# Optimization experiments

Hardware: AMD Instinct MI355X
Metric: run time of the kernel (lower is better)

The kernel has to match this reference:

```python
import jax, jax.numpy as jnp
import numpy as np

K = 3
NUM_STEP_COMBO = 5
BN_EPS = 1e-5


def setup_inputs() -> dict:
    key = jax.random.key(0)
    ks = jax.random.split(key, 10)
    N, E, D, H, O, G = 100000, 1600000, 48, 128, 12, 64
    x = jax.random.normal(ks[0], (N, D), dtype=jnp.float32)
    edge_index = jax.random.randint(ks[1], (2, E), 0, N, dtype=jnp.int64)
    batch = jnp.sort(jax.random.randint(ks[2], (N,), 0, G, dtype=jnp.int64))
    # ChebConv params: one [D, D] weight per Chebyshev order, shared bias
    W = jax.random.normal(ks[3], (K, D, D), dtype=jnp.float32) * 0.1
    b = jnp.zeros((D,), dtype=jnp.float32)
    gamma = jnp.ones((D,), dtype=jnp.float32)
    beta = jnp.zeros((D,), dtype=jnp.float32)
    W1 = jax.random.normal(ks[4], (D, H), dtype=jnp.float32) * 0.1
    b1 = jnp.zeros((H,), dtype=jnp.float32)
    W2 = jax.random.normal(ks[5], (H, O), dtype=jnp.float32) * 0.1
    b2 = jnp.zeros((O,), dtype=jnp.float32)
    return {"x": x, "edge_index": edge_index, "batch": batch, "num_graphs": 64,
            "W": W, "b": b, "gamma": gamma, "beta": beta,
            "W1": W1, "b1": b1, "W2": W2, "b2": b2}


def cheb_conv(x, row, col, W, b):
    # PyG ChebConv, sym norm, lambda_max=2 => L_hat = -D^{-1/2} A D^{-1/2}
    N = x.shape[0]
    deg = jax.ops.segment_sum(jnp.ones_like(row, dtype=x.dtype), row, num_segments=N)
    dinv = jnp.where(deg > 0, jax.lax.rsqrt(jnp.maximum(deg, 1.0)), 0.0)
    norm = (-dinv[row] * dinv[col])[:, None]  # [E,1] edge weights of L_hat

    def lhat(v):  # sparse matvec: gather neighbors, scale, scatter-add
        return jax.ops.segment_sum(norm * v[col], row, num_segments=N)

    Tx0 = x
    Tx1 = lhat(x)
    out = Tx0 @ W[0] + Tx1 @ W[1]
    Txkm2, Txkm1 = Tx0, Tx1
    for k in range(2, W.shape[0]):
        Txk = 2.0 * lhat(Txkm1) - Txkm2
        out = out + Txk @ W[k]
        Txkm2, Txkm1 = Txkm1, Txk
    return out + b


def reference(x, edge_index, batch, num_graphs, W, b, gamma, beta, W1, b1, W2, b2):
    row, col = edge_index[0], edge_index[1]
    N = x.shape[0]
    out = x
    for _ in range(NUM_STEP_COMBO):
        t = jax.nn.relu(cheb_conv(out, row, col, W, b))
        # BatchNorm1d (training-mode stats over all nodes, biased var)
        mean = jnp.mean(t, axis=0)
        var = jnp.mean((t - mean) ** 2, axis=0)
        t = gamma * (t - mean) * jax.lax.rsqrt(var + BN_EPS) + beta
        # graph_max_pool: per-node max over incoming neighbor features
        m = jax.ops.segment_max(t[col], row, num_segments=N)
        out = jnp.where(jnp.isneginf(m), 0.0, m)  # empty segments -> 0
    g = jax.ops.segment_sum(out, batch, num_segments=num_graphs)  # global_add_pool
    h = jax.nn.relu(g @ W1 + b1)
    return h @ W2 + b2
```

## Files before the change

### kernel.cpp

```cpp
#include <hip/hip_runtime.h>
#include <hip/hip_bf16.h>

#define D 48
#define GNUM 64
#define HDIM 128
#define ODIM 12
#define BN_EPS 1e-5f

typedef _Float16 half4v __attribute__((ext_vector_type(4)));
typedef float f32x4 __attribute__((ext_vector_type(4)));

#define MFMA16(a, b, c) __builtin_amdgcn_mfma_f32_16x16x16f16((a), (b), (c), 0, 0, 0)


__global__ __launch_bounds__(256) void k_deg(const int* __restrict__ row, int* __restrict__ deg, int E) {
    int e = blockIdx.x * 256 + threadIdx.x;
    if (e < E) atomicAdd(&deg[row[e]], 1);
}

__global__ __launch_bounds__(256) void k_scan1(const int* __restrict__ deg, int* __restrict__ incl,
                                               int* __restrict__ bsum, float* __restrict__ dinv, int N) {
    __shared__ int s[256];
    int i = blockIdx.x * 256 + threadIdx.x;
    int d = (i < N) ? deg[i] : 0;
    if (i < N) dinv[i] = d > 0 ? rsqrtf((float)d) : 0.f;
    s[threadIdx.x] = d;
    __syncthreads();
    for (int off = 1; off < 256; off <<= 1) {
        int t = (threadIdx.x >= off) ? s[threadIdx.x - off] : 0;
        __syncthreads();
        s[threadIdx.x] += t;
        __syncthreads();
    }
    if (i < N) incl[i] = s[threadIdx.x];
    if (threadIdx.x == 255) bsum[blockIdx.x] = s[255];
}

__global__ __launch_bounds__(512) void k_scan2(int* __restrict__ bsum, int nb) {
    __shared__ int s[512];
    int t = threadIdx.x;
    s[t] = (t < nb) ? bsum[t] : 0;
    __syncthreads();
    for (int off = 1; off < 512; off <<= 1) {
        int v = (t >= off) ? s[t - off] : 0;
        __syncthreads();
        s[t] += v;
        __syncthreads();
    }
    if (t < nb) bsum[t] = s[t];
}

__global__ __launch_bounds__(256) void k_scan3(const int* __restrict__ incl, const int* __restrict__ bsum,
                                               int* __restrict__ rowptr, int N) {
    int i = blockIdx.x * 256 + threadIdx.x;
    if (i < N) {
        int add = (blockIdx.x > 0) ? bsum[blockIdx.x - 1] : 0;
        rowptr[i + 1] = incl[i] + add;
    }
    if (i == 0) rowptr[0] = 0;
}

__global__ __launch_bounds__(256) void k_fill(const int* __restrict__ row, const int* __restrict__ col,
                                              const int* __restrict__ rowptr, int* __restrict__ fillc,
                                              const float* __restrict__ dinv, int2* __restrict__ epair,
                                              int E, int N) {
    int part = blockIdx.x & 7;
    int sub = blockIdx.x >> 3;
    int nsub = (int)(gridDim.x >> 3);
    int lo = (int)(((long long)N * part) >> 3);
    int hi = (int)(((long long)N * (part + 1)) >> 3);
    for (int e = sub * 256 + threadIdx.x; e < E; e += nsub * 256) {
        int r = __builtin_nontemporal_load(&row[e]);
        if (r >= lo && r < hi) {
            int c = __builtin_nontemporal_load(&col[e]);
            int p = rowptr[r] + atomicAdd(&fillc[r], 1);
            epair[p] = make_int2(c, __float_as_int(dinv[c]));
        }
    }
}

__global__ __launch_bounds__(256) void k_cvt(const float* __restrict__ x, _Float16* __restrict__ xh, int n4) {
    int i = blockIdx.x * 256 + threadIdx.x;
    if (i < n4) {
        float4 v = ((const float4*)x)[i];
        half4v h;
        h.x = (_Float16)v.x; h.y = (_Float16)v.y; h.z = (_Float16)v.z; h.w = (_Float16)v.w;
        ((half4v*)xh)[i] = h;
    }
}

__global__ __launch_bounds__(256) void k_wb(const float* __restrict__ W, _Float16* __restrict__ WB) {
    int idx = blockIdx.x * 256 + threadIdx.x;
    if (idx < 27 * 64) {
        int lane = idx & 63, ct = idx >> 6;
        int c = ct / 3, tl = ct % 3;
        int col = lane & 15, kg = lane >> 4;
        half4v h;
#pragma unroll
        for (int j = 0; j < 4; ++j) h[j] = (_Float16)W[(c * 16 + kg * 4 + j) * 48 + tl * 16 + col];
        *(half4v*)(WB + (size_t)idx * 4) = h;
    }
}


__global__ __launch_bounds__(256) void k_lhat(const _Float16* __restrict__ cur, const int* __restrict__ rowptr,
                                              const int2* __restrict__ epair, const float* __restrict__ dinv,
                                              _Float16* __restrict__ tx1, int N) {
    int lane = threadIdx.x & 63;
    int i = (blockIdx.x * 256 + threadIdx.x) >> 6;
    if (i >= N) return;
    int q = lane & 15, slot = lane >> 4;
    int qc = q < 12 ? q : 11;
    int s = rowptr[i], e = rowptr[i + 1];
    float a0 = 0.f, a1 = 0.f, a2 = 0.f, a3 = 0.f;
    int p = s + slot;
    for (; p + 12 < e; p += 16) {
        int2 e0 = epair[p], e1 = epair[p + 4], e2 = epair[p + 8], e3 = epair[p + 12];
        half4v h0 = *(const half4v*)(cur + (size_t)e0.x * D + qc * 4);
        half4v h1 = *(const half4v*)(cur + (size_t)e1.x * D + qc * 4);
        half4v h2 = *(const half4v*)(cur + (size_t)e2.x * D + qc * 4);
        half4v h3 = *(const half4v*)(cur + (size_t)e3.x * D + qc * 4);
        float w0 = __int_as_float(e0.y), w1 = __int_as_float(e1.y);
        float w2 = __int_as_float(e2.y), w3 = __int_as_float(e3.y);
        a0 += w0 * (float)h0.x + w1 * (float)h1.x + w2 * (float)h2.x + w3 * (float)h3.x;
        a1 += w0 * (float)h0.y + w1 * (float)h1.y + w2 * (float)h2.y + w3 * (float)h3.y;
        a2 += w0 * (float)h0.z + w1 * (float)h1.z + w2 * (float)h2.z + w3 * (float)h3.z;
        a3 += w0 * (float)h0.w + w1 * (float)h1.w + w2 * (float)h2.w + w3 * (float)h3.w;
    }
    for (; p < e; p += 4) {
        int2 ea = epair[p];
        float wa = __int_as_float(ea.y);
        half4v ha = *(const half4v*)(cur + (size_t)ea.x * D + qc * 4);
        a0 += wa * (float)ha.x; a1 += wa * (float)ha.y; a2 += wa * (float)ha.z; a3 += wa * (float)ha.w;
    }
    a0 += __shfl_xor(a0, 16); a1 += __shfl_xor(a1, 16); a2 += __shfl_xor(a2, 16); a3 += __shfl_xor(a3, 16);
    a0 += __shfl_xor(a0, 32); a1 += __shfl_xor(a1, 32); a2 += __shfl_xor(a2, 32); a3 += __shfl_xor(a3, 32);
    if (lane < 12) {
        float sc = -dinv[i];
        half4v o;
        o.x = (_Float16)(sc * a0); o.y = (_Float16)(sc * a1);
        o.z = (_Float16)(sc * a2); o.w = (_Float16)(sc * a3);
        *(half4v*)(tx1 + (size_t)i * D + lane * 4) = o;
    }
}

__global__ __launch_bounds__(256) void k_gather2(const _Float16* __restrict__ tx0, const _Float16* __restrict__ tx1,
                                                 const int* __restrict__ rowptr, const int2* __restrict__ epair,
                                                 const float* __restrict__ dinv, _Float16* __restrict__ tx2, int N) {
    int lane = threadIdx.x & 63;
    int i = (blockIdx.x * 256 + threadIdx.x) >> 6;
    if (i >= N) return;
    int q = lane & 15, slot = lane >> 4;
    int qc = q < 12 ? q : 11;
    int s = rowptr[i], e = rowptr[i + 1];
    float a0 = 0.f, a1 = 0.f, a2 = 0.f, a3 = 0.f;
    int p = s + slot;
    for (; p + 12 < e; p += 16) {
        int2 e0 = epair[p], e1 = epair[p + 4], e2 = epair[p + 8], e3 = epair[p + 12];
        half4v h0 = *(const half4v*)(tx1 + (size_t)e0.x * D + qc * 4);
        half4v h1 = *(const half4v*)(tx1 + (size_t)e1.x * D + qc * 4);
        half4v h2 = *(const half4v*)(tx1 + (size_t)e2.x * D + qc * 4);
        half4v h3 = *(const half4v*)(tx1 + (size_t)e3.x * D + qc * 4);
        float w0 = __int_as_float(e0.y), w1 = __int_as_float(e1.y);
        float w2 = __int_as_float(e2.y), w3 = __int_as_float(e3.y);
        a0 += w0 * (float)h0.x + w1 * (float)h1.x + w2 * (float)h2.x + w3 * (float)h3.x;
        a1 += w0 * (float)h0.y + w1 * (float)h1.y + w2 * (float)h2.y + w3 * (float)h3.y;
        a2 += w0 * (float)h0.z + w1 * (float)h1.z + w2 * (float)h2.z + w3 * (float)h3.z;
        a3 += w0 * (float)h0.w + w1 * (float)h1.w + w2 * (float)h2.w + w3 * (float)h3.w;
    }
    for (; p < e; p += 4) {
        int2 ea = epair[p];
        float wa = __int_as_float(ea.y);
        half4v ha = *(const half4v*)(tx1 + (size_t)ea.x * D + qc * 4);
        a0 += wa * (float)ha.x; a1 += wa * (float)ha.y; a2 += wa * (float)ha.z; a3 += wa * (float)ha.w;
    }
    a0 += __shfl_xor(a0, 16); a1 += __shfl_xor(a1, 16); a2 += __shfl_xor(a2, 16); a3 += __shfl_xor(a3, 16);
    a0 += __shfl_xor(a0, 32); a1 += __shfl_xor(a1, 32); a2 += __shfl_xor(a2, 32); a3 += __shfl_xor(a3, 32);
    if (lane < 12) {
        float sc = -2.f * dinv[i];
        half4v h0 = *(const half4v*)(tx0 + (size_t)i * D + lane * 4);
        half4v o;
        o.x = (_Float16)(sc * a0 - (float)h0.x); o.y = (_Float16)(sc * a1 - (float)h0.y);
        o.z = (_Float16)(sc * a2 - (float)h0.z); o.w = (_Float16)(sc * a3 - (float)h0.w);
        *(half4v*)(tx2 + (size_t)i * D + lane * 4) = o;
    }
}


__global__ __launch_bounds__(256) void k_dense(const _Float16* __restrict__ tx0, const _Float16* __restrict__ tx1,
                                               const _Float16* __restrict__ tx2, const _Float16* __restrict__ WB,
                                               const float* __restrict__ b, _Float16* __restrict__ tbuf,
                                               float* __restrict__ bnst, int N) {
    __shared__ float bns[2 * D];
    int t = threadIdx.x;
    if (t < 2 * D) bns[t] = 0.f;
    __syncthreads();

    int lane = t & 63, wave = t >> 6;
    int node0 = (blockIdx.x * 4 + wave) * 16;
    if (node0 < N) {
        int col = lane & 15, kg = lane >> 4;
        int nodeA = node0 + col;
        bool inA = nodeA < N;
        const _Float16* __restrict__ Xs[3] = {tx0 + (size_t)nodeA * D, tx1 + (size_t)nodeA * D,
                                              tx2 + (size_t)nodeA * D};
        f32x4 acc0 = {}, acc1 = {}, acc2 = {};
#pragma unroll
        for (int c = 0; c < 9; ++c) {
            half4v a = {};
            if (inA) a = *(const half4v*)(Xs[c / 3] + (c % 3) * 16 + kg * 4);
            half4v b0 = *(const half4v*)(WB + ((size_t)(c * 3 + 0) * 64 + lane) * 4);
            half4v b1 = *(const half4v*)(WB + ((size_t)(c * 3 + 1) * 64 + lane) * 4);
            half4v b2 = *(const half4v*)(WB + ((size_t)(c * 3 + 2) * 64 + lane) * 4);
            acc0 = MFMA16(a, b0, acc0);
            acc1 = MFMA16(a, b1, acc1);
            acc2 = MFMA16(a, b2, acc2);
        }
        float bc0 = b[col], bc1 = b[16 + col], bc2 = b[32 + col];
        float s0 = 0.f, q0 = 0.f, s1 = 0.f, q1 = 0.f, s2 = 0.f, q2 = 0.f;
#pragma unroll
        for (int i = 0; i < 4; ++i) {
            int nd = node0 + kg * 4 + i;
            float v0 = fmaxf(acc0[i] + bc0, 0.f);
            float v1 = fmaxf(acc1[i] + bc1, 0.f);
            float v2 = fmaxf(acc2[i] + bc2, 0.f);
            if (nd < N) {
                _Float16* o = tbuf + (size_t)nd * D;
                o[col] = (_Float16)v0;
                o[16 + col] = (_Float16)v1;
                o[32 + col] = (_Float16)v2;
                s0 += v0; q0 += v0 * v0;
                s1 += v1; q1 += v1 * v1;
                s2 += v2; q2 += v2 * v2;
            }
        }
        s0 += __shfl_xor(s0, 16); s0 += __shfl_xor(s0, 32);
        q0 += __shfl_xor(q0, 16); q0 += __shfl_xor(q0, 32);
        s1 += __shfl_xor(s1, 16); s1 += __shfl_xor(s1, 32);
        q1 += __shfl_xor(q1, 16); q1 += __shfl_xor(q1, 32);
        s2 += __shfl_xor(s2, 16); s2 += __shfl_xor(s2, 32);
        q2 += __shfl_xor(q2, 16); q2 += __shfl_xor(q2, 32);
        if (lane < 16) {
            atomicAdd(&bns[col], s0);      atomicAdd(&bns[D + col], q0);
            atomicAdd(&bns[16 + col], s1); atomicAdd(&bns[D + 16 + col], q1);
            atomicAdd(&bns[32 + col], s2); atomicAdd(&bns[D + 32 + col], q2);
        }
    }
    __syncthreads();
    if (t < 2 * D) atomicAdd(&bnst[t], bns[t]);
}


__global__ __launch_bounds__(256) void k_pool(const _Float16* __restrict__ tbuf, const int* __restrict__ rowptr,
                                              const int2* __restrict__ epair, const float* __restrict__ bnst,
                                              const float* __restrict__ gamma, const float* __restrict__ beta,
                                              float Ninv, _Float16* __restrict__ outh, int N) {
    __shared__ float ssL[2 * D];
    int t = threadIdx.x;
    if (t < D) {
        float mean = bnst[t] * Ninv;
        float var = fmaxf(bnst[D + t] * Ninv - mean * mean, 0.f);
        float sc = gamma[t] * rsqrtf(var + BN_EPS);
        ssL[t] = sc;
        ssL[D + t] = beta[t] - mean * sc;
    }
    __syncthreads();
    int lane = t & 63;
    int i = (blockIdx.x * 256 + t) >> 6;
    if (i >= N) return;
    int q = lane & 15, slot = lane >> 4;
    int qc = q < 12 ? q : 11;
    int s = rowptr[i], e = rowptr[i + 1];
    float m0 = -3.4e38f, m1 = -3.4e38f, m2 = -3.4e38f, m3 = -3.4e38f;
    float n0 = 3.4e38f, n1 = 3.4e38f, n2 = 3.4e38f, n3 = 3.4e38f;
    int p = s + slot;
    for (; p + 12 < e; p += 16) {
        int c0 = epair[p].x, c1 = epair[p + 4].x, c2 = epair[p + 8].x, c3 = epair[p + 12].x;
        half4v h0 = *(const half4v*)(tbuf + (size_t)c0 * D + qc * 4);
        half4v h1 = *(const half4v*)(tbuf + (size_t)c1 * D + qc * 4);
        half4v h2 = *(const half4v*)(tbuf + (size_t)c2 * D + qc * 4);
        half4v h3 = *(const half4v*)(tbuf + (size_t)c3 * D + qc * 4);
        float x00 = (float)h0.x, x01 = (float)h0.y, x02 = (float)h0.z, x03 = (float)h0.w;
        float x10 = (float)h1.x, x11 = (float)h1.y, x12 = (float)h1.z, x13 = (float)h1.w;
        float x20 = (float)h2.x, x21 = (float)h2.y, x22 = (float)h2.z, x23 = (float)h2.w;
        float x30 = (float)h3.x, x31 = (float)h3.y, x32 = (float)h3.z, x33 = (float)h3.w;
        m0 = fmaxf(m0, fmaxf(fmaxf(x00, x10), fmaxf(x20, x30)));
        m1 = fmaxf(m1, fmaxf(fmaxf(x01, x11), fmaxf(x21, x31)));
        m2 = fmaxf(m2, fmaxf(fmaxf(x02, x12), fmaxf(x22, x32)));
        m3 = fmaxf(m3, fmaxf(fmaxf(x03, x13), fmaxf(x23, x33)));
        n0 = fminf(n0, fminf(fminf(x00, x10), fminf(x20, x30)));
        n1 = fminf(n1, fminf(fminf(x01, x11), fminf(x21, x31)));
        n2 = fminf(n2, fminf(fminf(x02, x12), fminf(x22, x32)));
        n3 = fminf(n3, fminf(fminf(x03, x13), fminf(x23, x33)));
    }
    for (; p < e; p += 4) {
        int ca = epair[p].x;
        half4v ha = *(const half4v*)(tbuf + (size_t)ca * D + qc * 4);
        float a0 = (float)ha.x, a1 = (float)ha.y, a2 = (float)ha.z, a3 = (float)ha.w;
        m0 = fmaxf(m0, a0); m1 = fmaxf(m1, a1); m2 = fmaxf(m2, a2); m3 = fmaxf(m3, a3);
        n0 = fminf(n0, a0); n1 = fminf(n1, a1); n2 = fminf(n2, a2); n3 = fminf(n3, a3);
    }
    m0 = fmaxf(m0, __shfl_xor(m0, 16)); m1 = fmaxf(m1, __shfl_xor(m1, 16));
    m2 = fmaxf(m2, __shfl_xor(m2, 16)); m3 = fmaxf(m3, __shfl_xor(m3, 16));
    m0 = fmaxf(m0, __shfl_xor(m0, 32)); m1 = fmaxf(m1, __shfl_xor(m1, 32));
    m2 = fmaxf(m2, __shfl_xor(m2, 32)); m3 = fmaxf(m3, __shfl_xor(m3, 32));
    n0 = fminf(n0, __shfl_xor(n0, 16)); n1 = fminf(n1, __shfl_xor(n1, 16));
    n2 = fminf(n2, __shfl_xor(n2, 16)); n3 = fminf(n3, __shfl_xor(n3, 16));
    n0 = fminf(n0, __shfl_xor(n0, 32)); n1 = fminf(n1, __shfl_xor(n1, 32));
    n2 = fminf(n2, __shfl_xor(n2, 32)); n3 = fminf(n3, __shfl_xor(n3, 32));
    if (lane < 12) {
        float4 sc = *(const float4*)(ssL + lane * 4);
        float4 sh = *(const float4*)(ssL + D + lane * 4);
        half4v o;
        if (s == e) {
            o.x = (_Float16)0.f; o.y = (_Float16)0.f; o.z = (_Float16)0.f; o.w = (_Float16)0.f;
        } else {
            float v0 = (sc.x >= 0.f) ? sc.x * m0 + sh.x : sc.x * n0 + sh.x;
            float v1 = (sc.y >= 0.f) ? sc.y * m1 + sh.y : sc.y * n1 + sh.y;
            float v2 = (sc.z >= 0.f) ? sc.z * m2 + sh.z : sc.z * n2 + sh.z;
            float v3 = (sc.w >= 0.f) ? sc.w * m3 + sh.w : sc.w * n3 + sh.w;
            o.x = (_Float16)v0; o.y = (_Float16)v1; o.z = (_Float16)v2; o.w = (_Float16)v3;
        }
        *(half4v*)(outh + (size_t)i * D + lane * 4) = o;
    }
}


__global__ __launch_bounds__(256) void k_gpool(const _Float16* __restrict__ outh, const int* __restrict__ batch,
                                               float* __restrict__ g, int N, int chunk) {
    int lane = threadIdx.x & 63;
    int wid = (blockIdx.x * 256 + threadIdx.x) >> 6;
    int start = wid * chunk;
    if (start >= N || lane >= 12) return;
    int end = start + chunk;
    if (end > N) end = N;
    int curb = batch[start];
    float a0 = 0.f, a1 = 0.f, a2 = 0.f, a3 = 0.f;
    for (int i = start; i < end; ++i) {
        int bi = batch[i];
        if (bi != curb) {
            atomicAdd(&g[curb * D + lane * 4 + 0], a0); atomicAdd(&g[curb * D + lane * 4 + 1], a1);
            atomicAdd(&g[curb * D + lane * 4 + 2], a2); atomicAdd(&g[curb * D + lane * 4 + 3], a3);
            curb = bi; a0 = a1 = a2 = a3 = 0.f;
        }
        half4v h = *(const half4v*)(outh + (size_t)i * D + lane * 4);
        a0 += (float)h.x; a1 += (float)h.y; a2 += (float)h.z; a3 += (float)h.w;
    }
    atomicAdd(&g[curb * D + lane * 4 + 0], a0); atomicAdd(&g[curb * D + lane * 4 + 1], a1);
    atomicAdd(&g[curb * D + lane * 4 + 2], a2); atomicAdd(&g[curb * D + lane * 4 + 3], a3);
}

__global__ __launch_bounds__(256) void k_mlp(const float* __restrict__ g, const float* __restrict__ W1,
                                             const float* __restrict__ b1, const float* __restrict__ W2,
                                             const float* __restrict__ b2, float* __restrict__ out) {
    __shared__ float gL[GNUM * D];
    __shared__ float hL[GNUM * HDIM];
    __shared__ float W1L[D * HDIM];
    int t = threadIdx.x;
    for (int i = t; i < GNUM * D; i += 256) gL[i] = g[i];
    for (int i = t; i < D * HDIM; i += 256) W1L[i] = W1[i];
    __syncthreads();
    for (int i = t; i < GNUM * HDIM; i += 256) {
        int gi = i >> 7, hj = i & 127;
        float a = b1[hj];
        for (int k = 0; k < D; ++k) a += gL[gi * D + k] * W1L[k * HDIM + hj];
        hL[i] = fmaxf(a, 0.f);
    }
    __syncthreads();
    for (int i = t; i < GNUM * ODIM; i += 256) {
        int gi = i / ODIM, oj = i % ODIM;
        float a = b2[oj];
        for (int k = 0; k < HDIM; ++k) a += hL[gi * HDIM + k] * W2[k * ODIM + oj];
        out[i] = a;
    }
}


extern "C" void kernel_launch(void* const* d_in, const int* in_sizes, int n_in,
                              void* d_out, int out_size, void* d_ws, size_t ws_size,
                              hipStream_t stream) {
    const float* x     = (const float*)d_in[0];
    const int*   ei    = (const int*)d_in[1];
    const int*   batch = (const int*)d_in[2];
    const float* W     = (const float*)d_in[4];
    const float* b     = (const float*)d_in[5];
    const float* gamma = (const float*)d_in[6];
    const float* beta  = (const float*)d_in[7];
    const float* W1    = (const float*)d_in[8];
    const float* b1    = (const float*)d_in[9];
    const float* W2    = (const float*)d_in[10];
    const float* b2    = (const float*)d_in[11];

    int N = in_sizes[0] / D;
    int E = in_sizes[1] / 2;
    const int* row = ei;
    const int* col = ei + E;

    char* w = (char*)d_ws;
    auto alloc = [&](size_t bytes) { char* p = w; w += (bytes + 255) & ~(size_t)255; return p; };
    int*       deg     = (int*)alloc((size_t)N * 4);
    float*     dinv    = (float*)alloc((size_t)N * 4);
    int*       fillc   = (int*)alloc((size_t)N * 4);
    int*       incl    = (int*)alloc((size_t)N * 4);
    int*       bsum    = (int*)alloc(4096);
    int*       rowptr  = (int*)alloc((size_t)(N + 1) * 4);
    int2*      epair   = (int2*)alloc((size_t)E * 8);
    _Float16*  xh      = (_Float16*)alloc((size_t)N * D * 2 + 64);
    _Float16*  tx1h    = (_Float16*)alloc((size_t)N * D * 2 + 64);
    _Float16*  tx2h    = (_Float16*)alloc((size_t)N * D * 2 + 64);
    _Float16*  tbufh   = (_Float16*)alloc((size_t)N * D * 2 + 64);
    _Float16*  outh    = (_Float16*)alloc((size_t)N * D * 2 + 64);
    _Float16*  WB      = (_Float16*)alloc(27 * 64 * 4 * 2);
    float*     bnstats = (float*)alloc(5 * 2 * D * 4);
    float*     g       = (float*)alloc((size_t)GNUM * D * 4);

    (void)hipMemsetAsync(deg, 0, (size_t)N * 4, stream);
    (void)hipMemsetAsync(fillc, 0, (size_t)N * 4, stream);
    (void)hipMemsetAsync(bnstats, 0, 5 * 2 * D * 4, stream);
    (void)hipMemsetAsync(g, 0, (size_t)GNUM * D * 4, stream);

    int nbE = (E + 255) / 256;
    int nbN = (N + 255) / 256;

    k_deg<<<nbE, 256, 0, stream>>>(row, deg, E);
    k_scan1<<<nbN, 256, 0, stream>>>(deg, incl, bsum, dinv, N);
    k_scan2<<<1, 512, 0, stream>>>(bsum, nbN);
    k_scan3<<<nbN, 256, 0, stream>>>(incl, bsum, rowptr, N);
    k_fill<<<2048, 256, 0, stream>>>(row, col, rowptr, fillc, dinv, epair, E, N);
    int n4 = N * D / 4;
    k_cvt<<<(n4 + 255) / 256, 256, 0, stream>>>(x, xh, n4);
    k_wb<<<7, 256, 0, stream>>>(W, WB);

    int nbWave = (N * 64 + 255) / 256;
    int nbDense = (((N + 15) / 16) + 3) / 4;
    float Ninv = 1.f / (float)N;
    const _Float16* cur = xh;
    for (int step = 0; step < 5; ++step) {
        float* bnst = bnstats + step * 2 * D;
        k_lhat<<<nbWave, 256, 0, stream>>>(cur, rowptr, epair, dinv, tx1h, N);
        k_gather2<<<nbWave, 256, 0, stream>>>(cur, tx1h, rowptr, epair, dinv, tx2h, N);
        k_dense<<<nbDense, 256, 0, stream>>>(cur, tx1h, tx2h, WB, b, tbufh, bnst, N);
        k_pool<<<nbWave, 256, 0, stream>>>(tbufh, rowptr, epair, bnst, gamma, beta, Ninv, outh, N);
        cur = outh;
    }

    int chunk = 32;
    int nwaves = (N + chunk - 1) / chunk;
    int nbG = (nwaves * 64 + 255) / 256;
    k_gpool<<<nbG, 256, 0, stream>>>(outh, batch, g, N, chunk);
    k_mlp<<<1, 256, 0, stream>>>(g, W1, b1, W2, b2, (float*)d_out);
}
```

Measured before the change: 1.342 ms.

## Build CSR via bucketed two-pass scatter instead of 8-way partitioned fill

```diff
diff --git a/kernel.cpp b/kernel.cpp
--- a/kernel.cpp
+++ b/kernel.cpp
@@ -60,22 +60,69 @@
     if (i == 0) rowptr[0] = 0;
 }
 
-__global__ __launch_bounds__(256) void k_fill(const int* __restrict__ row, const int* __restrict__ col,
-                                              const int* __restrict__ rowptr, int* __restrict__ fillc,
-                                              const float* __restrict__ dinv, int2* __restrict__ epair,
-                                              int E, int N) {
+
+__global__ __launch_bounds__(256) void k_bcnt(const int* __restrict__ row, int* __restrict__ bcnt, int E) {
+    __shared__ int h[256];
+    h[threadIdx.x] = 0;
+    __syncthreads();
     int part = blockIdx.x & 7;
-    int sub = blockIdx.x >> 3;
-    int nsub = (int)(gridDim.x >> 3);
-    int lo = (int)(((long long)N * part) >> 3);
-    int hi = (int)(((long long)N * (part + 1)) >> 3);
-    for (int e = sub * 256 + threadIdx.x; e < E; e += nsub * 256) {
-        int r = __builtin_nontemporal_load(&row[e]);
-        if (r >= lo && r < hi) {
-            int c = __builtin_nontemporal_load(&col[e]);
-            int p = rowptr[r] + atomicAdd(&fillc[r], 1);
-            epair[p] = make_int2(c, __float_as_int(dinv[c]));
-        }
+    for (int e = blockIdx.x * 256 + threadIdx.x; e < E; e += gridDim.x * 256)
+        atomicAdd(&h[row[e] >> 9], 1);
+    __syncthreads();
+    int c = h[threadIdx.x];
+    if (c) atomicAdd(&bcnt[(threadIdx.x << 3) | part], c);
+}
+
+__global__ __launch_bounds__(512) void k_bscan(const int* __restrict__ bcnt, int* __restrict__ bstart,
+                                               int* __restrict__ bfill, int M) {
+    __shared__ int s[512];
+    int t = threadIdx.x;
+    int vals[4];
+    int acc = 0;
+#pragma unroll
+    for (int k = 0; k < 4; ++k) {
+        int i = t * 4 + k;
+        vals[k] = (i < M) ? bcnt[i] : 0;
+        acc += vals[k];
+    }
+    s[t] = acc;
+    __syncthreads();
+    for (int off = 1; off < 512; off <<= 1) {
+        int v = (t >= off) ? s[t - off] : 0;
+        __syncthreads();
+        s[t] += v;
+        __syncthreads();
+    }
+    int ex = s[t] - acc;
+#pragma unroll
+    for (int k = 0; k < 4; ++k) {
+        int i = t * 4 + k;
+        if (i < M) { bstart[i] = ex; bfill[i] = ex; }
+        ex += vals[k];
+    }
+}
+
+__global__ __launch_bounds__(256) void k_bscat(const int* __restrict__ row, const int* __restrict__ col,
+                                               int* __restrict__ bfill, int2* __restrict__ ebuf, int E) {
+    int part = blockIdx.x & 7;
+    for (int e = blockIdx.x * 256 + threadIdx.x; e < E; e += gridDim.x * 256) {
+        int r = row[e], c = col[e];
+        int pos = atomicAdd(&bfill[((r >> 9) << 3) | part], 1);
+        ebuf[pos] = make_int2(r, c);
+    }
+}
+
+__global__ __launch_bounds__(256) void k_cfill(const int2* __restrict__ ebuf, const int* __restrict__ rowptr,
+                                               int* __restrict__ fillc, const float* __restrict__ dinv,
+                                               int2* __restrict__ epair, int E) {
+    int part = blockIdx.x >> 8;
+    int sub = blockIdx.x & 255;
+    int lo = (int)((long long)E * part / 8);
+    int hi = (int)((long long)E * (part + 1) / 8);
+    for (int e = lo + sub * 256 + threadIdx.x; e < hi; e += 256 * 256) {
+        int2 rc = ebuf[e];
+        int pos = rowptr[rc.x] + atomicAdd(&fillc[rc.x], 1);
+        epair[pos] = make_int2(rc.y, __float_as_int(dinv[rc.y]));
     }
 }
 
@@ -404,6 +451,9 @@
     int*       incl    = (int*)alloc((size_t)N * 4);
     int*       bsum    = (int*)alloc(4096);
     int*       rowptr  = (int*)alloc((size_t)(N + 1) * 4);
+    int*       bcnt    = (int*)alloc(2048 * 4);
+    int*       bstart  = (int*)alloc(2048 * 4);
+    int*       bfill   = (int*)alloc(2048 * 4);
     int2*      epair   = (int2*)alloc((size_t)E * 8);
     _Float16*  xh      = (_Float16*)alloc((size_t)N * D * 2 + 64);
     _Float16*  tx1h    = (_Float16*)alloc((size_t)N * D * 2 + 64);
@@ -413,20 +463,27 @@
     _Float16*  WB      = (_Float16*)alloc(27 * 64 * 4 * 2);
     float*     bnstats = (float*)alloc(5 * 2 * D * 4);
     float*     g       = (float*)alloc((size_t)GNUM * D * 4);
+    int2*      ebuf    = (int2*)tbufh;
 
     (void)hipMemsetAsync(deg, 0, (size_t)N * 4, stream);
     (void)hipMemsetAsync(fillc, 0, (size_t)N * 4, stream);
+    (void)hipMemsetAsync(bcnt, 0, 2048 * 4, stream);
     (void)hipMemsetAsync(bnstats, 0, 5 * 2 * D * 4, stream);
     (void)hipMemsetAsync(g, 0, (size_t)GNUM * D * 4, stream);
 
     int nbE = (E + 255) / 256;
     int nbN = (N + 255) / 256;
+    int NB = (N + 511) >> 9;
+    int M = NB * 8;
 
     k_deg<<<nbE, 256, 0, stream>>>(row, deg, E);
     k_scan1<<<nbN, 256, 0, stream>>>(deg, incl, bsum, dinv, N);
     k_scan2<<<1, 512, 0, stream>>>(bsum, nbN);
     k_scan3<<<nbN, 256, 0, stream>>>(incl, bsum, rowptr, N);
-    k_fill<<<2048, 256, 0, stream>>>(row, col, rowptr, fillc, dinv, epair, E, N);
+    k_bcnt<<<2048, 256, 0, stream>>>(row, bcnt, E);
+    k_bscan<<<1, 512, 0, stream>>>(bcnt, bstart, bfill, M);
+    k_bscat<<<2048, 256, 0, stream>>>(row, col, bfill, ebuf, E);
+    k_cfill<<<2048, 256, 0, stream>>>(ebuf, rowptr, fillc, dinv, epair, E);
     int n4 = N * D / 4;
     k_cvt<<<(n4 + 255) / 256, 256, 0, stream>>>(x, xh, n4);
     k_wb<<<7, 256, 0, stream>>>(W, WB);
```

Measured after the change: 1.619 ms. 20.6% more time.

## Widen gather loads to 16-byte half8 with 8 edge slots per wave

Applied to the files above, without the earlier changes.

```diff
diff --git a/kernel.cpp b/kernel.cpp
--- a/kernel.cpp
+++ b/kernel.cpp
@@ -8,6 +8,7 @@
 #define BN_EPS 1e-5f
 
 typedef _Float16 half4v __attribute__((ext_vector_type(4)));
+typedef _Float16 half8v __attribute__((ext_vector_type(8)));
 typedef float f32x4 __attribute__((ext_vector_type(4)));
 
 #define MFMA16(a, b, c) __builtin_amdgcn_mfma_f32_16x16x16f16((a), (b), (c), 0, 0, 0)
@@ -63,16 +64,16 @@
 __global__ __launch_bounds__(256) void k_fill(const int* __restrict__ row, const int* __restrict__ col,
                                               const int* __restrict__ rowptr, int* __restrict__ fillc,
                                               const float* __restrict__ dinv, int2* __restrict__ epair,
-                                              int E, int N) {
+                                              int e0, int e1, int N) {
     int part = blockIdx.x & 7;
     int sub = blockIdx.x >> 3;
     int nsub = (int)(gridDim.x >> 3);
     int lo = (int)(((long long)N * part) >> 3);
     int hi = (int)(((long long)N * (part + 1)) >> 3);
-    for (int e = sub * 256 + threadIdx.x; e < E; e += nsub * 256) {
-        int r = __builtin_nontemporal_load(&row[e]);
+    for (int e = e0 + sub * 256 + threadIdx.x; e < e1; e += nsub * 256) {
+        int r = row[e];
         if (r >= lo && r < hi) {
-            int c = __builtin_nontemporal_load(&col[e]);
+            int c = col[e];
             int p = rowptr[r] + atomicAdd(&fillc[r], 1);
             epair[p] = make_int2(c, __float_as_int(dinv[c]));
         }
@@ -103,44 +104,61 @@
 }
 
 
+#define GATHER_REDUCE8(A)                                             \
+    A##0 += __shfl_xor(A##0, 8);  A##1 += __shfl_xor(A##1, 8);        \
+    A##2 += __shfl_xor(A##2, 8);  A##3 += __shfl_xor(A##3, 8);        \
+    A##4 += __shfl_xor(A##4, 8);  A##5 += __shfl_xor(A##5, 8);        \
+    A##6 += __shfl_xor(A##6, 8);  A##7 += __shfl_xor(A##7, 8);        \
+    A##0 += __shfl_xor(A##0, 16); A##1 += __shfl_xor(A##1, 16);       \
+    A##2 += __shfl_xor(A##2, 16); A##3 += __shfl_xor(A##3, 16);       \
+    A##4 += __shfl_xor(A##4, 16); A##5 += __shfl_xor(A##5, 16);       \
+    A##6 += __shfl_xor(A##6, 16); A##7 += __shfl_xor(A##7, 16);       \
+    A##0 += __shfl_xor(A##0, 32); A##1 += __shfl_xor(A##1, 32);       \
+    A##2 += __shfl_xor(A##2, 32); A##3 += __shfl_xor(A##3, 32);       \
+    A##4 += __shfl_xor(A##4, 32); A##5 += __shfl_xor(A##5, 32);       \
+    A##6 += __shfl_xor(A##6, 32); A##7 += __shfl_xor(A##7, 32);
+
 __global__ __launch_bounds__(256) void k_lhat(const _Float16* __restrict__ cur, const int* __restrict__ rowptr,
                                               const int2* __restrict__ epair, const float* __restrict__ dinv,
                                               _Float16* __restrict__ tx1, int N) {
     int lane = threadIdx.x & 63;
     int i = (blockIdx.x * 256 + threadIdx.x) >> 6;
     if (i >= N) return;
-    int q = lane & 15, slot = lane >> 4;
-    int qc = q < 12 ? q : 11;
+    int slot = lane >> 3, j = lane & 7;
+    int jb = (j < 6 ? j : 5) * 8;
     int s = rowptr[i], e = rowptr[i + 1];
-    float a0 = 0.f, a1 = 0.f, a2 = 0.f, a3 = 0.f;
+    float a0 = 0.f, a1 = 0.f, a2 = 0.f, a3 = 0.f, a4 = 0.f, a5 = 0.f, a6 = 0.f, a7 = 0.f;
     int p = s + slot;
-    for (; p + 12 < e; p += 16) {
-        int2 e0 = epair[p], e1 = epair[p + 4], e2 = epair[p + 8], e3 = epair[p + 12];
-        half4v h0 = *(const half4v*)(cur + (size_t)e0.x * D + qc * 4);
-        half4v h1 = *(const half4v*)(cur + (size_t)e1.x * D + qc * 4);
-        half4v h2 = *(const half4v*)(cur + (size_t)e2.x * D + qc * 4);
-        half4v h3 = *(const half4v*)(cur + (size_t)e3.x * D + qc * 4);
-        float w0 = __int_as_float(e0.y), w1 = __int_as_float(e1.y);
-        float w2 = __int_as_float(e2.y), w3 = __int_as_float(e3.y);
-        a0 += w0 * (float)h0.x + w1 * (float)h1.x + w2 * (float)h2.x + w3 * (float)h3.x;
-        a1 += w0 * (float)h0.y + w1 * (float)h1.y + w2 * (float)h2.y + w3 * (float)h3.y;
-        a2 += w0 * (float)h0.z + w1 * (float)h1.z + w2 * (float)h2.z + w3 * (float)h3.z;
-        a3 += w0 * (float)h0.w + w1 * (float)h1.w + w2 * (float)h2.w + w3 * (float)h3.w;
-    }
-    for (; p < e; p += 4) {
+    for (; p + 8 < e; p += 16) {
+        int2 ea = epair[p], eb = epair[p + 8];
+        half8v ha = *(const half8v*)(cur + (size_t)ea.x * D + jb);
+        half8v hb = *(const half8v*)(cur + (size_t)eb.x * D + jb);
+        float wa = __int_as_float(ea.y), wb = __int_as_float(eb.y);
+        a0 += wa * (float)ha[0] + wb * (float)hb[0];
+        a1 += wa * (float)ha[1] + wb * (float)hb[1];
+        a2 += wa * (float)ha[2] + wb * (float)hb[2];
+        a3 += wa * (float)ha[3] + wb * (float)hb[3];
+        a4 += wa * (float)ha[4] + wb * (float)hb[4];
+        a5 += wa * (float)ha[5] + wb * (float)hb[5];
+        a6 += wa * (float)ha[6] + wb * (float)hb[6];
+        a7 += wa * (float)ha[7] + wb * (float)hb[7];
+    }
+    if (p < e) {
         int2 ea = epair[p];
+        half8v ha = *(const half8v*)(cur + (size_t)ea.x * D + jb);
         float wa = __int_as_float(ea.y);
-        half4v ha = *(const half4v*)(cur + (size_t)ea.x * D + qc * 4);
-        a0 += wa * (float)ha.x; a1 += wa * (float)ha.y; a2 += wa * (float)ha.z; a3 += wa * (float)ha.w;
-    }
-    a0 += __shfl_xor(a0, 16); a1 += __shfl_xor(a1, 16); a2 += __shfl_xor(a2, 16); a3 += __shfl_xor(a3, 16);
-    a0 += __shfl_xor(a0, 32); a1 += __shfl_xor(a1, 32); a2 += __shfl_xor(a2, 32); a3 += __shfl_xor(a3, 32);
-    if (lane < 12) {
+        a0 += wa * (float)ha[0]; a1 += wa * (float)ha[1]; a2 += wa * (float)ha[2]; a3 += wa * (float)ha[3];
+        a4 += wa * (float)ha[4]; a5 += wa * (float)ha[5]; a6 += wa * (float)ha[6]; a7 += wa * (float)ha[7];
+    }
+    GATHER_REDUCE8(a)
+    if (slot == 0 && j < 6) {
         float sc = -dinv[i];
-        half4v o;
-        o.x = (_Float16)(sc * a0); o.y = (_Float16)(sc * a1);
-        o.z = (_Float16)(sc * a2); o.w = (_Float16)(sc * a3);
-        *(half4v*)(tx1 + (size_t)i * D + lane * 4) = o;
+        half8v o;
+        o[0] = (_Float16)(sc * a0); o[1] = (_Float16)(sc * a1);
+        o[2] = (_Float16)(sc * a2); o[3] = (_Float16)(sc * a3);
+        o[4] = (_Float16)(sc * a4); o[5] = (_Float16)(sc * a5);
+        o[6] = (_Float16)(sc * a6); o[7] = (_Float16)(sc * a7);
+        *(half8v*)(tx1 + (size_t)i * D + jb) = o;
     }
 }
 
@@ -150,39 +168,42 @@
     int lane = threadIdx.x & 63;
     int i = (blockIdx.x * 256 + threadIdx.x) >> 6;
     if (i >= N) return;
-    int q = lane & 15, slot = lane >> 4;
-    int qc = q < 12 ? q : 11;
+    int slot = lane >> 3, j = lane & 7;
+    int jb = (j < 6 ? j : 5) * 8;
     int s = rowptr[i], e = rowptr[i + 1];
-    float a0 = 0.f, a1 = 0.f, a2 = 0.f, a3 = 0.f;
+    float a0 = 0.f, a1 = 0.f, a2 = 0.f, a3 = 0.f, a4 = 0.f, a5 = 0.f, a6 = 0.f, a7 = 0.f;
     int p = s + slot;
-    for (; p + 12 < e; p += 16) {
-        int2 e0 = epair[p], e1 = epair[p + 4], e2 = epair[p + 8], e3 = epair[p + 12];
-        half4v h0 = *(const half4v*)(tx1 + (size_t)e0.x * D + qc * 4);
-        half4v h1 = *(const half4v*)(tx1 + (size_t)e1.x * D + qc * 4);
-        half4v h2 = *(const half4v*)(tx1 + (size_t)e2.x * D + qc * 4);
-        half4v h3 = *(const half4v*)(tx1 + (size_t)e3.x * D + qc * 4);
-        float w0 = __int_as_float(e0.y), w1 = __int_as_float(e1.y);
-        float w2 = __int_as_float(e2.y), w3 = __int_as_float(e3.y);
-        a0 += w0 * (float)h0.x + w1 * (float)h1.x + w2 * (float)h2.x + w3 * (float)h3.x;
-        a1 += w0 * (float)h0.y + w1 * (float)h1.y + w2 * (float)h2.y + w3 * (float)h3.y;
-        a2 += w0 * (float)h0.z + w1 * (float)h1.z + w2 * (float)h2.z + w3 * (float)h3.z;
-        a3 += w0 * (float)h0.w + w1 * (float)h1.w + w2 * (float)h2.w + w3 * (float)h3.w;
-    }
-    for (; p < e; p += 4) {
+    for (; p + 8 < e; p += 16) {
+        int2 ea = epair[p], eb = epair[p + 8];
+        half8v ha = *(const half8v*)(tx1 + (size_t)ea.x * D + jb);
+        half8v hb = *(const half8v*)(tx1 + (size_t)eb.x * D + jb);
+        float wa = __int_as_float(ea.y), wb = __int_as_float(eb.y);
+        a0 += wa * (float)ha[0] + wb * (float)hb[0];
+        a1 += wa * (float)ha[1] + wb * (float)hb[1];
+        a2 += wa * (float)ha[2] + wb * (float)hb[2];
+        a3 += wa * (float)ha[3] + wb * (float)hb[3];
+        a4 += wa * (float)ha[4] + wb * (float)hb[4];
+        a5 += wa * (float)ha[5] + wb * (float)hb[5];
+        a6 += wa * (float)ha[6] + wb * (float)hb[6];
+        a7 += wa * (float)ha[7] + wb * (float)hb[7];
+    }
+    if (p < e) {
         int2 ea = epair[p];
+        half8v ha = *(const half8v*)(tx1 + (size_t)ea.x * D + jb);
         float wa = __int_as_float(ea.y);
-        half4v ha = *(const half4v*)(tx1 + (size_t)ea.x * D + qc * 4);
-        a0 += wa * (float)ha.x; a1 += wa * (float)ha.y; a2 += wa * (float)ha.z; a3 += wa * (float)ha.w;
-    }
-    a0 += __shfl_xor(a0, 16); a1 += __shfl_xor(a1, 16); a2 += __shfl_xor(a2, 16); a3 += __shfl_xor(a3, 16);
-    a0 += __shfl_xor(a0, 32); a1 += __shfl_xor(a1, 32); a2 += __shfl_xor(a2, 32); a3 += __shfl_xor(a3, 32);
-    if (lane < 12) {
+        a0 += wa * (float)ha[0]; a1 += wa * (float)ha[1]; a2 += wa * (float)ha[2]; a3 += wa * (float)ha[3];
+        a4 += wa * (float)ha[4]; a5 += wa * (float)ha[5]; a6 += wa * (float)ha[6]; a7 += wa * (float)ha[7];
+    }
+    GATHER_REDUCE8(a)
+    if (slot == 0 && j < 6) {
         float sc = -2.f * dinv[i];
-        half4v h0 = *(const half4v*)(tx0 + (size_t)i * D + lane * 4);
-        half4v o;
-        o.x = (_Float16)(sc * a0 - (float)h0.x); o.y = (_Float16)(sc * a1 - (float)h0.y);
-        o.z = (_Float16)(sc * a2 - (float)h0.z); o.w = (_Float16)(sc * a3 - (float)h0.w);
-        *(half4v*)(tx2 + (size_t)i * D + lane * 4) = o;
+        half8v h0 = *(const half8v*)(tx0 + (size_t)i * D + jb);
+        half8v o;
+        o[0] = (_Float16)(sc * a0 - (float)h0[0]); o[1] = (_Float16)(sc * a1 - (float)h0[1]);
+        o[2] = (_Float16)(sc * a2 - (float)h0[2]); o[3] = (_Float16)(sc * a3 - (float)h0[3]);
+        o[4] = (_Float16)(sc * a4 - (float)h0[4]); o[5] = (_Float16)(sc * a5 - (float)h0[5]);
+        o[6] = (_Float16)(sc * a6 - (float)h0[6]); o[7] = (_Float16)(sc * a7 - (float)h0[7]);
+        *(half8v*)(tx2 + (size_t)i * D + jb) = o;
     }
 }
 
@@ -268,60 +289,73 @@
     int lane = t & 63;
     int i = (blockIdx.x * 256 + t) >> 6;
     if (i >= N) return;
-    int q = lane & 15, slot = lane >> 4;
-    int qc = q < 12 ? q : 11;
+    int slot = lane >> 3, j = lane & 7;
+    int jb = (j < 6 ? j : 5) * 8;
     int s = rowptr[i], e = rowptr[i + 1];
     float m0 = -3.4e38f, m1 = -3.4e38f, m2 = -3.4e38f, m3 = -3.4e38f;
+    float m4 = -3.4e38f, m5 = -3.4e38f, m6 = -3.4e38f, m7 = -3.4e38f;
     float n0 = 3.4e38f, n1 = 3.4e38f, n2 = 3.4e38f, n3 = 3.4e38f;
+    float n4 = 3.4e38f, n5 = 3.4e38f, n6 = 3.4e38f, n7 = 3.4e38f;
     int p = s + slot;
-    for (; p + 12 < e; p += 16) {
-        int c0 = epair[p].x, c1 = epair[p + 4].x, c2 = epair[p + 8].x, c3 = epair[p + 12].x;
-        half4v h0 = *(const half4v*)(tbuf + (size_t)c0 * D + qc * 4);
-        half4v h1 = *(const half4v*)(tbuf + (size_t)c1 * D + qc * 4);
-        half4v h2 = *(const half4v*)(tbuf + (size_t)c2 * D + qc * 4);
-        half4v h3 = *(const half4v*)(tbuf + (size_t)c3 * D + qc * 4);
-        float x00 = (float)h0.x, x01 = (float)h0.y, x02 = (float)h0.z, x03 = (float)h0.w;
-        float x10 = (float)h1.x, x11 = (float)h1.y, x12 = (float)h1.z, x13 = (float)h1.w;
-        float x20 = (float)h2.x, x21 = (float)h2.y, x22 = (float)h2.z, x23 = (float)h2.w;
-        float x30 = (float)h3.x, x31 = (float)h3.y, x32 = (float)h3.z, x33 = (float)h3.w;
-        m0 = fmaxf(m0, fmaxf(fmaxf(x00, x10), fmaxf(x20, x30)));
-        m1 = fmaxf(m1, fmaxf(fmaxf(x01, x11), fmaxf(x21, x31)));
-        m2 = fmaxf(m2, fmaxf(fmaxf(x02, x12), fmaxf(x22, x32)));
-        m3 = fmaxf(m3, fmaxf(fmaxf(x03, x13), fmaxf(x23, x33)));
-        n0 = fminf(n0, fminf(fminf(x00, x10), fminf(x20, x30)));
-        n1 = fminf(n1, fminf(fminf(x01, x11), fminf(x21, x31)));
-        n2 = fminf(n2, fminf(fminf(x02, x12), fminf(x22, x32)));
-        n3 = fminf(n3, fminf(fminf(x03, x13), fminf(x23, x33)));
-    }
-    for (; p < e; p += 4) {
+    for (; p + 8 < e; p += 16) {
+        int ca = epair[p].x, cb = epair[p + 8].x;
+        half8v ha = *(const half8v*)(tbuf + (size_t)ca * D + jb);
+        half8v hb = *(const half8v*)(tbuf + (size_t)cb * D + jb);
+        float x0 = (float)ha[0], y0 = (float)hb[0], x1 = (float)ha[1], y1 = (float)hb[1];
+        float x2 = (float)ha[2], y2 = (float)hb[2], x3 = (float)ha[3], y3 = (float)hb[3];
+        float x4 = (float)ha[4], y4 = (float)hb[4], x5 = (float)ha[5], y5 = (float)hb[5];
+        float x6 = (float)ha[6], y6 = (float)hb[6], x7 = (float)ha[7], y7 = (float)hb[7];
+        m0 = fmaxf(m0, fmaxf(x0, y0)); m1 = fmaxf(m1, fmaxf(x1, y1));
+        m2 = fmaxf(m2, fmaxf(x2, y2)); m3 = fmaxf(m3, fmaxf(x3, y3));
+        m4 = fmaxf(m4, fmaxf(x4, y4)); m5 = fmaxf(m5, fmaxf(x5, y5));
+        m6 = fmaxf(m6, fmaxf(x6, y6)); m7 = fmaxf(m7, fmaxf(x7, y7));
+        n0 = fminf(n0, fminf(x0, y0)); n1 = fminf(n1, fminf(x1, y1));
+        n2 = fminf(n2, fminf(x2, y2)); n3 = fminf(n3, fminf(x3, y3));
+        n4 = fminf(n4, fminf(x4, y4)); n5 = fminf(n5, fminf(x5, y5));
+        n6 = fminf(n6, fminf(x6, y6)); n7 = fminf(n7, fminf(x7, y7));
+    }
+    if (p < e) {
         int ca = epair[p].x;
-        half4v ha = *(const half4v*)(tbuf + (size_t)ca * D + qc * 4);
-        float a0 = (float)ha.x, a1 = (float)ha.y, a2 = (float)ha.z, a3 = (float)ha.w;
-        m0 = fmaxf(m0, a0); m1 = fmaxf(m1, a1); m2 = fmaxf(m2, a2); m3 = fmaxf(m3, a3);
-        n0 = fminf(n0, a0); n1 = fminf(n1, a1); n2 = fminf(n2, a2); n3 = fminf(n3, a3);
-    }
-    m0 = fmaxf(m0, __shfl_xor(m0, 16)); m1 = fmaxf(m1, __shfl_xor(m1, 16));
-    m2 = fmaxf(m2, __shfl_xor(m2, 16)); m3 = fmaxf(m3, __shfl_xor(m3, 16));
-    m0 = fmaxf(m0, __shfl_xor(m0, 32)); m1 = fmaxf(m1, __shfl_xor(m1, 32));
-    m2 = fmaxf(m2, __shfl_xor(m2, 32)); m3 = fmaxf(m3, __shfl_xor(m3, 32));
-    n0 = fminf(n0, __shfl_xor(n0, 16)); n1 = fminf(n1, __shfl_xor(n1, 16));
-    n2 = fminf(n2, __shfl_xor(n2, 16)); n3 = fminf(n3, __shfl_xor(n3, 16));
-    n0 = fminf(n0, __shfl_xor(n0, 32)); n1 = fminf(n1, __shfl_xor(n1, 32));
-    n2 = fminf(n2, __shfl_xor(n2, 32)); n3 = fminf(n3, __shfl_xor(n3, 32));
-    if (lane < 12) {
-        float4 sc = *(const float4*)(ssL + lane * 4);
-        float4 sh = *(const float4*)(ssL + D + lane * 4);
-        half4v o;
+        half8v ha = *(const half8v*)(tbuf + (size_t)ca * D + jb);
+        float x0 = (float)ha[0], x1 = (float)ha[1], x2 = (float)ha[2], x3 = (float)ha[3];
+        float x4 = (float)ha[4], x5 = (float)ha[5], x6 = (float)ha[6], x7 = (float)ha[7];
+        m0 = fmaxf(m0, x0); m1 = fmaxf(m1, x1); m2 = fmaxf(m2, x2); m3 = fmaxf(m3, x3);
+        m4 = fmaxf(m4, x4); m5 = fmaxf(m5, x5); m6 = fmaxf(m6, x6); m7 = fmaxf(m7, x7);
+        n0 = fminf(n0, x0); n1 = fminf(n1, x1); n2 = fminf(n2, x2); n3 = fminf(n3, x3);
+        n4 = fminf(n4, x4); n5 = fminf(n5, x5); n6 = fminf(n6, x6); n7 = fminf(n7, x7);
+    }
+#define PRED8(A, OP)                                                  \
+    A##0 = OP(A##0, __shfl_xor(A##0, 8));  A##1 = OP(A##1, __shfl_xor(A##1, 8));   \
+    A##2 = OP(A##2, __shfl_xor(A##2, 8));  A##3 = OP(A##3, __shfl_xor(A##3, 8));   \
+    A##4 = OP(A##4, __shfl_xor(A##4, 8));  A##5 = OP(A##5, __shfl_xor(A##5, 8));   \
+    A##6 = OP(A##6, __shfl_xor(A##6, 8));  A##7 = OP(A##7, __shfl_xor(A##7, 8));   \
+    A##0 = OP(A##0, __shfl_xor(A##0, 16)); A##1 = OP(A##1, __shfl_xor(A##1, 16));  \
+    A##2 = OP(A##2, __shfl_xor(A##2, 16)); A##3 = OP(A##3, __shfl_xor(A##3, 16));  \
+    A##4 = OP(A##4, __shfl_xor(A##4, 16)); A##5 = OP(A##5, __shfl_xor(A##5, 16));  \
+    A##6 = OP(A##6, __shfl_xor(A##6, 16)); A##7 = OP(A##7, __shfl_xor(A##7, 16));  \
+    A##0 = OP(A##0, __shfl_xor(A##0, 32)); A##1 = OP(A##1, __shfl_xor(A##1, 32));  \
+    A##2 = OP(A##2, __shfl_xor(A##2, 32)); A##3 = OP(A##3, __shfl_xor(A##3, 32));  \
+    A##4 = OP(A##4, __shfl_xor(A##4, 32)); A##5 = OP(A##5, __shfl_xor(A##5, 32));  \
+    A##6 = OP(A##6, __shfl_xor(A##6, 32)); A##7 = OP(A##7, __shfl_xor(A##7, 32));
+    PRED8(m, fmaxf)
+    PRED8(n, fminf)
+#undef PRED8
+    if (slot == 0 && j < 6) {
+        half8v o;
         if (s == e) {
-            o.x = (_Float16)0.f; o.y = (_Float16)0.f; o.z = (_Float16)0.f; o.w = (_Float16)0.f;
+#pragma unroll
+            for (int k = 0; k < 8; ++k) o[k] = (_Float16)0.f;
         } else {
-            float v0 = (sc.x >= 0.f) ? sc.x * m0 + sh.x : sc.x * n0 + sh.x;
-            float v1 = (sc.y >= 0.f) ? sc.y * m1 + sh.y : sc.y * n1 + sh.y;
-            float v2 = (sc.z >= 0.f) ? sc.z * m2 + sh.z : sc.z * n2 + sh.z;
-            float v3 = (sc.w >= 0.f) ? sc.w * m3 + sh.w : sc.w * n3 + sh.w;
-            o.x = (_Float16)v0; o.y = (_Float16)v1; o.z = (_Float16)v2; o.w = (_Float16)v3;
-        }
-        *(half4v*)(outh + (size_t)i * D + lane * 4) = o;
+            float mm[8] = {m0, m1, m2, m3, m4, m5, m6, m7};
+            float nn[8] = {n0, n1, n2, n3, n4, n5, n6, n7};
+#pragma unroll
+            for (int k = 0; k < 8; ++k) {
+                float sc = ssL[jb + k], sh = ssL[D + jb + k];
+                float v = (sc >= 0.f) ? sc * mm[k] + sh : sc * nn[k] + sh;
+                o[k] = (_Float16)v;
+            }
+        }
+        *(half8v*)(outh + (size_t)i * D + jb) = o;
     }
 }
 
@@ -426,7 +460,10 @@
     k_scan1<<<nbN, 256, 0, stream>>>(deg, incl, bsum, dinv, N);
     k_scan2<<<1, 512, 0, stream>>>(bsum, nbN);
     k_scan3<<<nbN, 256, 0, stream>>>(incl, bsum, rowptr, N);
-    k_fill<<<2048, 256, 0, stream>>>(row, col, rowptr, fillc, dinv, epair, E, N);
+    int E3 = E / 3;
+    k_fill<<<2048, 256, 0, stream>>>(row, col, rowptr, fillc, dinv, epair, 0, E3, N);
+    k_fill<<<2048, 256, 0, stream>>>(row, col, rowptr, fillc, dinv, epair, E3, 2 * E3, N);
+    k_fill<<<2048, 256, 0, stream>>>(row, col, rowptr, fillc, dinv, epair, 2 * E3, E, N);
     int n4 = N * D / 4;
     k_cvt<<<(n4 + 255) / 256, 256, 0, stream>>>(x, xh, n4);
     k_wb<<<7, 256, 0, stream>>>(W, WB);
```

Result: faster. 1.272 ms (-5.2%).
